# Kernel tuning notes

Measured on AMD Instinct MI355X. Metric: run time of the kernel, lower is better.

The kernel has to match this reference:

```python
import jax, jax.numpy as jnp
import numpy as np

C = 1.0          # curvature args.c
ALPHA = 3.0      # self.alpha
MIN = 1e-15      # min_norm clamp (HGCN PoincareBall)
PROJ_EPS = 4e-3  # fp32 boundary eps (HGCN)


def _norm(x):
    return jnp.maximum(jnp.linalg.norm(x, axis=-1, keepdims=True), MIN)


def artanh(x):
    # clamp for fp32 stability (HGCN clamps to 1 - 1e-15; 1e-7 is the fp32 analogue)
    return jnp.arctanh(jnp.clip(x, -1.0 + 1e-7, 1.0 - 1e-7))


def proj(x, c):
    n = _norm(x)
    maxn = (1.0 - PROJ_EPS) / jnp.sqrt(c)
    return jnp.where(n > maxn, x / n * maxn, x)


def expmap0(u, c):
    sc = jnp.sqrt(c)
    n = _norm(u)
    return jnp.tanh(sc * n) * u / (sc * n)


def logmap0(p, c):
    sc = jnp.sqrt(c)
    n = _norm(p)
    return artanh(sc * n) * p / (sc * n)


def mobius_add(x, y, c):
    x2 = jnp.sum(x * x, axis=-1, keepdims=True)
    y2 = jnp.sum(y * y, axis=-1, keepdims=True)
    xy = jnp.sum(x * y, axis=-1, keepdims=True)
    num = (1.0 + 2.0 * c * xy + c * y2) * x + (1.0 - c * x2) * y
    den = 1.0 + 2.0 * c * xy + c * c * x2 * y2
    return num / jnp.maximum(den, MIN)


def mobius_matvec(m, x, c):
    sc = jnp.sqrt(c)
    xn = _norm(x)
    mx = x @ m.T                      # [..., out]
    mxn = _norm(mx)
    res = jnp.tanh(mxn / xn * artanh(sc * xn)) * mx / (mxn * sc)
    zero_rows = jnp.all(mx == 0.0, axis=-1, keepdims=True)
    return jnp.where(zero_rows, 0.0, res)


def hyp_linear(x, W, b, c):
    # dropout on weights is identity in eval mode
    mv = proj(mobius_matvec(W, x, c), c)
    hb = proj(expmap0(b[None, :], c), c)  # proj_tan0 is identity on Poincare ball
    return proj(mobius_add(mv, hb, c), c)


def setup_inputs() -> dict:
    key = jax.random.key(0)
    N, D, F = 8192, 128, 128
    ks = jax.random.split(key, 8)
    gain = np.sqrt(2.0 / (D + D)) * np.sqrt(2.0)  # xavier-like scale
    return {
        "idx": jnp.arange(N, dtype=jnp.int32),
        "dist_metrix": jnp.zeros((1,), dtype=jnp.float32),
        "x": jax.random.normal(ks[0], (N, F), dtype=jnp.float32),
        "emb1": jax.random.normal(ks[1], (N, D), dtype=jnp.float32),
        "emb2": jax.random.normal(ks[2], (N, D), dtype=jnp.float32),
        "W1": jax.random.normal(ks[3], (D, D), dtype=jnp.float32) * gain,
        "b1": jax.random.normal(ks[4], (D,), dtype=jnp.float32) * 0.01,
        "W2": jax.random.normal(ks[5], (D, D), dtype=jnp.float32) * gain,
        "b2": jax.random.normal(ks[6], (D,), dtype=jnp.float32) * 0.01,
    }


def reference(idx, dist_metrix, x, emb1, emb2, W1, b1, W2, b2):
    # node embeddings lifted to the Poincare ball (proj_tan0 is identity)
    nv1 = proj(expmap0(emb1[idx], C), C)
    nv2 = proj(expmap0(emb2[idx], C), C)
    nv1 = hyp_linear(nv1, W1, b1, C)
    nv2 = hyp_linear(nv2, W2, b2, C)
    # adjacency construction: a1 = nv2 @ nv1^T (mobius), a2 = nv1 @ nv2^T (mobius)
    a1 = mobius_matvec(nv1, nv2, C)   # [N, N]
    a2 = mobius_matvec(nv2, nv1, C)   # [N, N]
    a = mobius_add(a1, -a2, C)
    adj = jax.nn.relu(jnp.tanh(ALPHA * a))
    n = adj.shape[0]
    adj = adj + 1e-4 * jnp.eye(n, dtype=adj.dtype)
    # row-normalize (scipy round-trip in original == row-sum divide, inf -> 0)
    rs = jnp.sum(adj, axis=1, keepdims=True)
    adj = adj * jnp.where(rs == 0.0, 0.0, 1.0 / rs)
    # propagate features
    xt = logmap0(x, C)                       # [N, F]
    out = mobius_matvec(xt.T, adj, C)        # adj @ xt -> [N, F]
    out = logmap0(out, C)
    return out
```

## Files before the change

kernel.cpp:

```cpp
#include <hip/hip_runtime.h>
#include <hip/hip_bf16.h>


typedef __attribute__((ext_vector_type(8))) short short8;
typedef __attribute__((ext_vector_type(4))) float f32x4;

#define MAXN 0.996f

__device__ __forceinline__ float artanh_clip(float x) {
    x = fminf(x, 1.0f - 1e-7f);
    x = fmaxf(x, -1.0f + 1e-7f);
    return 0.5f * logf((1.0f + x) / (1.0f - x));
}

__device__ __forceinline__ float red8(float v) {
    v += __shfl_xor(v, 1);
    v += __shfl_xor(v, 2);
    v += __shfl_xor(v, 4);
    return v;
}

__device__ __forceinline__ float red64(float v) {
#pragma unroll
    for (int m = 1; m < 64; m <<= 1) v += __shfl_xor(v, m);
    return v;
}

__device__ __forceinline__ unsigned short f2bf(float f) {
    __hip_bfloat16 h = __float2bfloat16(f);
    return *reinterpret_cast<unsigned short*>(&h);
}

__device__ __forceinline__ float bf2f(unsigned short u) {
    __hip_bfloat16 h;
    *reinterpret_cast<unsigned short*>(&h) = u;
    return __bfloat162float(h);
}

__global__ void hb_kernel(const float* __restrict__ b1, const float* __restrict__ b2,
                          float* __restrict__ hbws) {
    const int l = threadIdx.x;
    for (int which = 0; which < 2; ++which) {
        const float* b = which ? b2 : b1;
        float e0 = b[l], e1 = b[l + 64];
        float n = fmaxf(sqrtf(red64(e0 * e0 + e1 * e1)), 1e-15f);
        float th = tanhf(n);
        float s0 = th / n;
        float u0 = e0 * s0, u1 = e1 * s0;
        float nu = fmaxf(sqrtf(red64(u0 * u0 + u1 * u1)), 1e-15f);
        float ps = (nu > MAXN) ? MAXN / nu : 1.0f;
        float h0 = u0 * ps, h1 = u1 * ps;
        float y2 = red64(h0 * h0 + h1 * h1);
        hbws[which * 128 + l] = h0;
        hbws[which * 128 + l + 64] = h1;
        if (l == 0) hbws[256 + which] = y2;
    }
}

__global__ __launch_bounds__(256) void prep_kernel(
    const int* __restrict__ idx,
    const float* __restrict__ emb1, const float* __restrict__ emb2,
    const float* __restrict__ W1, const float* __restrict__ W2,
    const float* __restrict__ hbws,
    unsigned short* __restrict__ nv1b, unsigned short* __restrict__ nv2b,
    float* __restrict__ xn1, float* __restrict__ xn2) {
    __shared__ __align__(16) float uL[32 * 132];
    __shared__ float mxL[32 * 132];
    __shared__ float xnL[32];
    __shared__ float hbL[128];

    const int which = blockIdx.y;
    const float* emb = which ? emb2 : emb1;
    const float* W = which ? W2 : W1;
    unsigned short* nvb = which ? nv2b : nv1b;
    float* xno = which ? xn2 : xn1;
    const float y2 = hbws[256 + which];

    const int tid = threadIdx.x;
    const int rblk = blockIdx.x * 32;
    if (tid < 128) hbL[tid] = hbws[which * 128 + tid];

    const int r = tid >> 3, s = tid & 7;
    const int row = rblk + r;
    const int src = idx[row];
    float ev[16];
    float p2 = 0.f;
#pragma unroll
    for (int kk = 0; kk < 16; ++kk) {
        float e = emb[src * 128 + s + kk * 8];
        ev[kk] = e;
        p2 += e * e;
    }
    float n2 = red8(p2);
    float n = fmaxf(sqrtf(n2), 1e-15f);
    float th = tanhf(n);
    float nu = fmaxf(th, 1e-15f);
    float ps = (nu > MAXN) ? (MAXN / nu) : 1.0f;
    float sc0 = (th / n) * ps;
#pragma unroll
    for (int kk = 0; kk < 16; ++kk) uL[r * 132 + s + kk * 8] = ev[kk] * sc0;
    if (s == 0) xnL[r] = fmaxf(nu * ps, 1e-15f);
    __syncthreads();

    const int o = tid & 127, rb = tid >> 7;
    float mxv[16];
#pragma unroll
    for (int rr = 0; rr < 16; ++rr) mxv[rr] = 0.f;
    for (int k4 = 0; k4 < 128; k4 += 4) {
        const float4 wv = *reinterpret_cast<const float4*>(&W[o * 128 + k4]);
#pragma unroll
        for (int rr = 0; rr < 16; ++rr) {
            const float4 uv = *reinterpret_cast<const float4*>(&uL[(rb + rr * 2) * 132 + k4]);
            mxv[rr] += uv.x * wv.x + uv.y * wv.y + uv.z * wv.z + uv.w * wv.w;
        }
    }
#pragma unroll
    for (int rr = 0; rr < 16; ++rr) mxL[(rb + rr * 2) * 132 + o] = mxv[rr];
    __syncthreads();

    float mx[16];
    float m2 = 0.f;
#pragma unroll
    for (int kk = 0; kk < 16; ++kk) {
        mx[kk] = mxL[r * 132 + s + kk * 8];
        m2 += mx[kk] * mx[kk];
    }
    float mxn = fmaxf(sqrtf(red8(m2)), 1e-15f);
    float xnv = xnL[r];
    float tt = tanhf(mxn / xnv * artanh_clip(xnv));
    float nres = fmaxf(tt, 1e-15f);
    float ps2 = (nres > MAXN) ? (MAXN / nres) : 1.0f;
    float s2 = (tt / mxn) * ps2;
    float mvn = nres * ps2;
    float x2 = mvn * mvn;
    float xyp = 0.f;
    float mv[16];
#pragma unroll
    for (int kk = 0; kk < 16; ++kk) {
        mv[kk] = mx[kk] * s2;
        xyp += mv[kk] * hbL[s + kk * 8];
    }
    float xy = red8(xyp);
    float cA = 1.f + 2.f * xy + y2;
    float cB = 1.f - x2;
    float rden = 1.f / fmaxf(1.f + 2.f * xy + x2 * y2, 1e-15f);
    float r2v[16];
    float q2 = 0.f;
#pragma unroll
    for (int kk = 0; kk < 16; ++kk) {
        float v = (cA * mv[kk] + cB * hbL[s + kk * 8]) * rden;
        r2v[kk] = v;
        q2 += v * v;
    }
    float nr2 = fmaxf(sqrtf(red8(q2)), 1e-15f);
    float ps3 = (nr2 > MAXN) ? (MAXN / nr2) : 1.0f;
#pragma unroll
    for (int kk = 0; kk < 16; ++kk) nvb[row * 128 + s + kk * 8] = f2bf(r2v[kk] * ps3);
    if (s == 0) xno[row] = fmaxf((nr2 > MAXN) ? MAXN : nr2, 1e-15f);
}

__global__ __launch_bounds__(256) void xt_kernel(const float* __restrict__ x,
                                                 unsigned short* __restrict__ xtT) {
    __shared__ float xv[32 * 132];
    const int tid = threadIdx.x;
    const int rblk = blockIdx.x * 32;
    const int r = tid >> 3, s = tid & 7;
    float ev[16];
    float p2 = 0.f;
#pragma unroll
    for (int kk = 0; kk < 16; ++kk) {
        float e = x[(rblk + r) * 128 + s + kk * 8];
        ev[kk] = e;
        p2 += e * e;
    }
    const float n = fmaxf(sqrtf(red8(p2)), 1e-15f);
    const float scl = artanh_clip(n) / n;
#pragma unroll
    for (int kk = 0; kk < 16; ++kk) xv[r * 132 + s + kk * 8] = ev[kk] * scl;
    __syncthreads();
    const int k = tid >> 1, h = tid & 1;
    short8 o0, o1;
#pragma unroll
    for (int j = 0; j < 8; ++j) o0[j] = (short)f2bf(xv[(h * 16 + j) * 132 + k]);
#pragma unroll
    for (int j = 0; j < 8; ++j) o1[j] = (short)f2bf(xv[(h * 16 + 8 + j) * 132 + k]);
    *reinterpret_cast<short8*>(&xtT[k * 8192 + rblk + h * 16]) = o0;
    *reinterpret_cast<short8*>(&xtT[k * 8192 + rblk + h * 16 + 8]) = o1;
}

__global__ __launch_bounds__(256) void gram_kernel(const unsigned short* __restrict__ nv1b,
                                                   const unsigned short* __restrict__ nv2b,
                                                   float* __restrict__ G) {
    __shared__ float Ab[64 * 33], Bb[64 * 33];
    const int tile = blockIdx.x, mat = blockIdx.y, kc = blockIdx.z;
    const int ta = (tile & 3) * 32, tb = (tile >> 2) * 32;
    const unsigned short* Am = (mat == 1) ? nv2b : nv1b;
    const unsigned short* Bm = (mat == 0) ? nv1b : nv2b;
    const int tid = threadIdx.x;
    const int oa = tid & 31, obb = (tid >> 5) * 4;
    float acc[4] = {0.f, 0.f, 0.f, 0.f};
    for (int sc = 0; sc < 16; ++sc) {
        const int r0 = kc * 1024 + sc * 64;
        for (int i0 = tid; i0 < 2048; i0 += 256) {
            int rr = i0 >> 5, cc = i0 & 31;
            Ab[rr * 33 + cc] = bf2f(Am[(r0 + rr) * 128 + ta + cc]);
            Bb[rr * 33 + cc] = bf2f(Bm[(r0 + rr) * 128 + tb + cc]);
        }
        __syncthreads();
#pragma unroll 4
        for (int rr = 0; rr < 64; ++rr) {
            float av = Ab[rr * 33 + oa];
#pragma unroll
            for (int i = 0; i < 4; ++i) acc[i] += av * Bb[rr * 33 + obb + i];
        }
        __syncthreads();
    }
#pragma unroll
    for (int i = 0; i < 4; ++i)
        atomicAdd(&G[mat * 16384 + (ta + oa) * 128 + tb + obb + i], acc[i]);
}

__global__ __launch_bounds__(256) void rowcoef_kernel(
    const float* __restrict__ G, const float* __restrict__ xn1, const float* __restrict__ xn2,
    const unsigned short* __restrict__ nv1b, const unsigned short* __restrict__ nv2b,
    float* __restrict__ P, float* __restrict__ Q) {
    __shared__ __align__(16) float v1L[32 * 132];
    __shared__ __align__(16) float v2L[32 * 132];
    __shared__ float tL[32 * 132];
    __shared__ float RCX[3][32];
    const int tid = threadIdx.x;
    const int rblk = blockIdx.x * 32;
    for (int i = tid; i < 4096; i += 256) {
        int r = i >> 7, c = i & 127;
        v1L[r * 132 + c] = bf2f(nv1b[(rblk + r) * 128 + c]);
        v2L[r * 132 + c] = bf2f(nv2b[(rblk + r) * 128 + c]);
    }
    __syncthreads();
    const int o = tid & 127, rb = tid >> 7;
    const int rA = tid >> 3, sA = tid & 7;
    for (int mat = 0; mat < 3; ++mat) {
        const float* vR = (mat == 0) ? v2L : v1L;
        const float* vL = (mat == 1) ? v1L : v2L;
        const float* Gm = G + mat * 16384;
        float tv[16];
#pragma unroll
        for (int rr = 0; rr < 16; ++rr) tv[rr] = 0.f;
        for (int k4 = 0; k4 < 128; k4 += 4) {
            const float4 gv = *reinterpret_cast<const float4*>(&Gm[o * 128 + k4]);
#pragma unroll
            for (int rr = 0; rr < 16; ++rr) {
                const float4 uv = *reinterpret_cast<const float4*>(&vR[(rb + rr * 2) * 132 + k4]);
                tv[rr] += uv.x * gv.x + uv.y * gv.y + uv.z * gv.z + uv.w * gv.w;
            }
        }
        __syncthreads();
#pragma unroll
        for (int rr = 0; rr < 16; ++rr) {
            int rw = rb + rr * 2;
            tL[rw * 132 + o] = vL[rw * 132 + o] * tv[rr];
        }
        __syncthreads();
        float p = 0.f;
#pragma unroll
        for (int kk = 0; kk < 16; ++kk) p += tL[rA * 132 + sA + kk * 8];
        p = red8(p);
        if (sA == 0) RCX[mat][rA] = p;
    }
    __syncthreads();
    if (tid < 32) {
        const int row = rblk + tid;
        const float R = RCX[0][tid], Cc = RCX[1][tid], X = RCX[2][tid];
        const float xn1v = xn1[row], xn2v = xn2[row];
        const float mxn1 = fmaxf(sqrtf(fmaxf(R, 0.f)), 1e-15f);
        const float t1 = tanhf(mxn1 / xn2v * artanh_clip(xn2v));
        const float f1 = t1 / mxn1;
        const float mxn2 = fmaxf(sqrtf(fmaxf(Cc, 0.f)), 1e-15f);
        const float t2 = tanhf(mxn2 / xn1v * artanh_clip(xn1v));
        const float f2 = t2 / mxn2;
        const float x2 = f1 * f1 * R, y2 = f2 * f2 * Cc;
        const float xy = -f1 * f2 * X;
        const float rden = 1.f / fmaxf(1.f + 2.f * xy + x2 * y2, 1e-15f);
        P[row] = (1.f + 2.f * xy + y2) * f1 * rden;
        Q[row] = -(1.f - x2) * f2 * rden;
    }
}

__global__ __launch_bounds__(512) void fused_kernel(
    const unsigned short* __restrict__ nv1b, const unsigned short* __restrict__ nv2b,
    const unsigned short* __restrict__ xtT,
    const float* __restrict__ P, const float* __restrict__ Q,
    float* __restrict__ U, float* __restrict__ rs, float* __restrict__ qs) {
    __shared__ float S1[32 * 132];
    __shared__ float S2[128 * 33];
    __shared__ __align__(16) unsigned short adjb[32 * 136];
    __shared__ float PL[32], QL[32];
    __shared__ int s2flag;

    const int tid = threadIdx.x;
    const int w = tid >> 6, l = tid & 63;
    const int iblk = blockIdx.x * 32;

    if (tid == 0) s2flag = 0;
    if (tid < 32) {
        PL[tid] = P[iblk + tid];
        QL[tid] = Q[iblk + tid];
    }
    __syncthreads();
    if (tid < 32 && fabsf(QL[tid]) > 1e-6f) atomicOr(&s2flag, 1);
    __syncthreads();
    const bool needS2 = (s2flag != 0);

    short8 areg[2][4];
#pragma unroll
    for (int tr = 0; tr < 2; ++tr)
#pragma unroll
        for (int kk = 0; kk < 4; ++kk)
            areg[tr][kk] = *reinterpret_cast<const short8*>(
                &nv2b[(iblk + tr * 16 + (l & 15)) * 128 + kk * 32 + (l >> 4) * 8]);

    const f32x4 zero4 = {0.f, 0.f, 0.f, 0.f};
    f32x4 accU[2];
    accU[0] = zero4;
    accU[1] = zero4;
    float rsA[4] = {0.f, 0.f, 0.f, 0.f};
    float qA[4] = {0.f, 0.f, 0.f, 0.f};

    auto computeS1 = [&](int jb) {
        const int jblk = jb * 128;
        f32x4 acc0 = zero4, acc1 = zero4;
#pragma unroll
        for (int kk = 0; kk < 4; ++kk) {
            short8 b = *reinterpret_cast<const short8*>(
                &nv1b[(jblk + w * 16 + (l & 15)) * 128 + kk * 32 + (l >> 4) * 8]);
            acc0 = __builtin_amdgcn_mfma_f32_16x16x32_bf16(areg[0][kk], b, acc0, 0, 0, 0);
            acc1 = __builtin_amdgcn_mfma_f32_16x16x32_bf16(areg[1][kk], b, acc1, 0, 0, 0);
        }
#pragma unroll
        for (int v = 0; v < 4; ++v) {
            S1[((l >> 4) * 4 + v) * 132 + w * 16 + (l & 15)] = acc0[v];
            S1[(16 + (l >> 4) * 4 + v) * 132 + w * 16 + (l & 15)] = acc1[v];
        }
        if (needS2) {
            f32x4 a20 = zero4, a21 = zero4;
#pragma unroll
            for (int kk = 0; kk < 4; ++kk) {
                short8 a2 = *reinterpret_cast<const short8*>(
                    &nv2b[(jblk + w * 16 + (l & 15)) * 128 + kk * 32 + (l >> 4) * 8]);
                short8 b20 = *reinterpret_cast<const short8*>(
                    &nv1b[(iblk + (l & 15)) * 128 + kk * 32 + (l >> 4) * 8]);
                short8 b21 = *reinterpret_cast<const short8*>(
                    &nv1b[(iblk + 16 + (l & 15)) * 128 + kk * 32 + (l >> 4) * 8]);
                a20 = __builtin_amdgcn_mfma_f32_16x16x32_bf16(a2, b20, a20, 0, 0, 0);
                a21 = __builtin_amdgcn_mfma_f32_16x16x32_bf16(a2, b21, a21, 0, 0, 0);
            }
#pragma unroll
            for (int v = 0; v < 4; ++v) {
                S2[(w * 16 + (l >> 4) * 4 + v) * 33 + (l & 15)] = a20[v];
                S2[(w * 16 + (l >> 4) * 4 + v) * 33 + 16 + (l & 15)] = a21[v];
            }
        }
    };

    computeS1(0);
    for (int jb = 0; jb < 64; ++jb) {
        const int jblk = jb * 128;
        __syncthreads();
#pragma unroll
        for (int k = 0; k < 4; ++k) {
            const int r = w + 8 * k;
            const float Pv = PL[r], Qv = QL[r];
#pragma unroll
            for (int h = 0; h < 2; ++h) {
                const int c = l + 64 * h;
                float a = Pv * S1[r * 132 + c];
                if (needS2) a += Qv * S2[c * 33 + r];
                float e = __expf(fminf(6.0f * a, 60.0f));
                float t = 1.0f - 2.0f / (e + 1.0f);
                float ad = (a > 0.0f) ? t : 0.0f;
                if (iblk + r == jblk + c) ad += 1e-4f;
                rsA[k] += ad;
                qA[k] += ad * ad;
                adjb[r * 136 + c] = f2bf(ad);
            }
        }
        __syncthreads();
#pragma unroll
        for (int kk = 0; kk < 4; ++kk) {
            short8 b = *reinterpret_cast<const short8*>(
                &xtT[(w * 16 + (l & 15)) * 8192 + jblk + kk * 32 + (l >> 4) * 8]);
#pragma unroll
            for (int tr = 0; tr < 2; ++tr) {
                short8 a = *reinterpret_cast<const short8*>(
                    &adjb[(tr * 16 + (l & 15)) * 136 + kk * 32 + (l >> 4) * 8]);
                accU[tr] = __builtin_amdgcn_mfma_f32_16x16x32_bf16(a, b, accU[tr], 0, 0, 0);
            }
        }
        if (jb + 1 < 64) computeS1(jb + 1);
    }

#pragma unroll
    for (int tr = 0; tr < 2; ++tr)
#pragma unroll
        for (int v = 0; v < 4; ++v)
            U[(iblk + tr * 16 + (l >> 4) * 4 + v) * 128 + w * 16 + (l & 15)] = accU[tr][v];
#pragma unroll
    for (int k = 0; k < 4; ++k) {
        float rsv = red64(rsA[k]);
        float qv = red64(qA[k]);
        if (l == 0) {
            rs[iblk + w + 8 * k] = rsv;
            qs[iblk + w + 8 * k] = qv;
        }
    }
}

__global__ void finalize_kernel(const float* __restrict__ U, const float* __restrict__ rs,
                                const float* __restrict__ qs, float* __restrict__ out) {
    const int row = blockIdx.x, l = threadIdx.x;
    const float u0 = U[row * 128 + l], u1 = U[row * 128 + 64 + l];
    const float rsv = rs[row];
    const float wv = (rsv == 0.f) ? 0.f : 1.f / rsv;
    const float m0 = u0 * wv, m1 = u1 * wv;
    const float mxn = fmaxf(sqrtf(red64(m0 * m0 + m1 * m1)), 1e-15f);
    const float xn = fmaxf(sqrtf(fmaxf(qs[row], 0.f)) * wv, 1e-15f);
    const float tt = tanhf(mxn / xn * artanh_clip(xn));
    const float nres = fmaxf(tt, 1e-15f);
    const float lsc = (tt / mxn) * (artanh_clip(nres) / nres);
    out[row * 128 + l] = m0 * lsc;
    out[row * 128 + 64 + l] = m1 * lsc;
}

extern "C" void kernel_launch(void* const* d_in, const int* in_sizes, int n_in,
                              void* d_out, int out_size, void* d_ws, size_t ws_size,
                              hipStream_t stream) {
    const int* idx = (const int*)d_in[0];
    const float* x = (const float*)d_in[2];
    const float* emb1 = (const float*)d_in[3];
    const float* emb2 = (const float*)d_in[4];
    const float* W1 = (const float*)d_in[5];
    const float* b1 = (const float*)d_in[6];
    const float* W2 = (const float*)d_in[7];
    const float* b2 = (const float*)d_in[8];
    float* out = (float*)d_out;
    char* ws = (char*)d_ws;

    unsigned short* nv1b = (unsigned short*)(ws + 0x000000);
    unsigned short* nv2b = (unsigned short*)(ws + 0x200000);
    unsigned short* xtT = (unsigned short*)(ws + 0x400000);
    float* G = (float*)(ws + 0x600000);
    float* hbws = (float*)(ws + 0x630000);
    float* xn1 = (float*)(ws + 0x630600);
    float* xn2 = (float*)(ws + 0x638600);
    float* P = (float*)(ws + 0x640600);
    float* Q = (float*)(ws + 0x648600);
    float* rs = (float*)(ws + 0x650600);
    float* qs = (float*)(ws + 0x658600);
    float* U = out;

    hipMemsetAsync(G, 0, 3 * 128 * 128 * sizeof(float), stream);
    hb_kernel<<<1, 64, 0, stream>>>(b1, b2, hbws);
    prep_kernel<<<dim3(256, 2), 256, 0, stream>>>(idx, emb1, emb2, W1, W2, hbws,
                                                  nv1b, nv2b, xn1, xn2);
    xt_kernel<<<256, 256, 0, stream>>>(x, xtT);
    gram_kernel<<<dim3(16, 3, 8), 256, 0, stream>>>(nv1b, nv2b, G);
    rowcoef_kernel<<<256, 256, 0, stream>>>(G, xn1, xn2, nv1b, nv2b, P, Q);
    fused_kernel<<<256, 512, 0, stream>>>(nv1b, nv2b, xtT, P, Q, U, rs, qs);
    finalize_kernel<<<8192, 64, 0, stream>>>(U, rs, qs, out);
    (void)in_sizes; (void)n_in; (void)out_size; (void)ws_size; (void)d_in;
}
```

Before: 400.5 us.

## Split fused adjacency kernel over column blocks and prescale nv2 by P

The fused adjacency-propagation kernel now runs on a 256x4 grid, with each block covering 16 of the 64 column blocks. Partial U, row-sum and square-sum results are combined with atomicAdd into buffers that are zeroed by memsets first. The row coefficient P is folded into a prescaled bf16 copy of nv2 built in rowcoef, so the inner loop drops one multiply. The Q term is merged into S1 directly instead of going through a separate S2 buffer, which frees shared memory. The tanh/relu is now computed with exp2 and rcp intrinsics, and the diagonal test only runs on diagonal tiles. The aim is to fill more of the GPU with 1024 blocks instead of 256, at the price of atomics, extra memsets, and an extra bf16 rounding of P*nv2.

```diff
diff --git a/kernel.cpp b/kernel.cpp
--- a/kernel.cpp
+++ b/kernel.cpp
@@ -223,11 +223,12 @@
 __global__ __launch_bounds__(256) void rowcoef_kernel(
     const float* __restrict__ G, const float* __restrict__ xn1, const float* __restrict__ xn2,
     const unsigned short* __restrict__ nv1b, const unsigned short* __restrict__ nv2b,
-    float* __restrict__ P, float* __restrict__ Q) {
+    float* __restrict__ P, float* __restrict__ Q, unsigned short* __restrict__ nv2p) {
     __shared__ __align__(16) float v1L[32 * 132];
     __shared__ __align__(16) float v2L[32 * 132];
     __shared__ float tL[32 * 132];
     __shared__ float RCX[3][32];
+    __shared__ float PshL[32];
     const int tid = threadIdx.x;
     const int rblk = blockIdx.x * 32;
     for (int i = tid; i < 4096; i += 256) {
@@ -280,31 +281,35 @@
         const float x2 = f1 * f1 * R, y2 = f2 * f2 * Cc;
         const float xy = -f1 * f2 * X;
         const float rden = 1.f / fmaxf(1.f + 2.f * xy + x2 * y2, 1e-15f);
-        P[row] = (1.f + 2.f * xy + y2) * f1 * rden;
+        const float Pv = (1.f + 2.f * xy + y2) * f1 * rden;
+        P[row] = Pv;
+        PshL[tid] = Pv;
         Q[row] = -(1.f - x2) * f2 * rden;
     }
-}
-
-__global__ __launch_bounds__(512) void fused_kernel(
-    const unsigned short* __restrict__ nv1b, const unsigned short* __restrict__ nv2b,
-    const unsigned short* __restrict__ xtT,
-    const float* __restrict__ P, const float* __restrict__ Q,
+    __syncthreads();
+    for (int i = tid; i < 4096; i += 256) {
+        int r = i >> 7, c = i & 127;
+        nv2p[(rblk + r) * 128 + c] = f2bf(PshL[r] * v2L[r * 132 + c]);
+    }
+}
+
+__global__ __launch_bounds__(512, 8) void fused_kernel(
+    const unsigned short* __restrict__ nv1b, const unsigned short* __restrict__ nv2p,
+    const unsigned short* __restrict__ nv2b, const unsigned short* __restrict__ xtT,
+    const float* __restrict__ Q,
     float* __restrict__ U, float* __restrict__ rs, float* __restrict__ qs) {
     __shared__ float S1[32 * 132];
-    __shared__ float S2[128 * 33];
     __shared__ __align__(16) unsigned short adjb[32 * 136];
-    __shared__ float PL[32], QL[32];
+    __shared__ float QL[32];
     __shared__ int s2flag;
 
     const int tid = threadIdx.x;
     const int w = tid >> 6, l = tid & 63;
     const int iblk = blockIdx.x * 32;
+    const int jb0 = blockIdx.y * 16;
 
     if (tid == 0) s2flag = 0;
-    if (tid < 32) {
-        PL[tid] = P[iblk + tid];
-        QL[tid] = Q[iblk + tid];
-    }
+    if (tid < 32) QL[tid] = Q[iblk + tid];
     __syncthreads();
     if (tid < 32 && fabsf(QL[tid]) > 1e-6f) atomicOr(&s2flag, 1);
     __syncthreads();
@@ -316,7 +321,7 @@
 #pragma unroll
         for (int kk = 0; kk < 4; ++kk)
             areg[tr][kk] = *reinterpret_cast<const short8*>(
-                &nv2b[(iblk + tr * 16 + (l & 15)) * 128 + kk * 32 + (l >> 4) * 8]);
+                &nv2p[(iblk + tr * 16 + (l & 15)) * 128 + kk * 32 + (l >> 4) * 8]);
 
     const f32x4 zero4 = {0.f, 0.f, 0.f, 0.f};
     f32x4 accU[2];
@@ -340,49 +345,58 @@
             S1[((l >> 4) * 4 + v) * 132 + w * 16 + (l & 15)] = acc0[v];
             S1[(16 + (l >> 4) * 4 + v) * 132 + w * 16 + (l & 15)] = acc1[v];
         }
+    };
+
+    auto s2merge = [&](int jb) {
+        const int jblk = jb * 128;
+        f32x4 a20 = zero4, a21 = zero4;
+#pragma unroll
+        for (int kk = 0; kk < 4; ++kk) {
+            short8 a2 = *reinterpret_cast<const short8*>(
+                &nv2b[(jblk + w * 16 + (l & 15)) * 128 + kk * 32 + (l >> 4) * 8]);
+            short8 b20 = *reinterpret_cast<const short8*>(
+                &nv1b[(iblk + (l & 15)) * 128 + kk * 32 + (l >> 4) * 8]);
+            short8 b21 = *reinterpret_cast<const short8*>(
+                &nv1b[(iblk + 16 + (l & 15)) * 128 + kk * 32 + (l >> 4) * 8]);
+            a20 = __builtin_amdgcn_mfma_f32_16x16x32_bf16(a2, b20, a20, 0, 0, 0);
+            a21 = __builtin_amdgcn_mfma_f32_16x16x32_bf16(a2, b21, a21, 0, 0, 0);
+        }
+        const int jloc = w * 16 + (l >> 4) * 4;
+        const int i0 = l & 15;
+#pragma unroll
+        for (int v = 0; v < 4; ++v) {
+            S1[i0 * 132 + jloc + v] += QL[i0] * a20[v];
+            S1[(i0 + 16) * 132 + jloc + v] += QL[i0 + 16] * a21[v];
+        }
+    };
+
+    computeS1(jb0);
+    for (int jb = jb0; jb < jb0 + 16; ++jb) {
+        const int jblk = jb * 128;
+        __syncthreads();
         if (needS2) {
-            f32x4 a20 = zero4, a21 = zero4;
-#pragma unroll
-            for (int kk = 0; kk < 4; ++kk) {
-                short8 a2 = *reinterpret_cast<const short8*>(
-                    &nv2b[(jblk + w * 16 + (l & 15)) * 128 + kk * 32 + (l >> 4) * 8]);
-                short8 b20 = *reinterpret_cast<const short8*>(
-                    &nv1b[(iblk + (l & 15)) * 128 + kk * 32 + (l >> 4) * 8]);
-                short8 b21 = *reinterpret_cast<const short8*>(
-                    &nv1b[(iblk + 16 + (l & 15)) * 128 + kk * 32 + (l >> 4) * 8]);
-                a20 = __builtin_amdgcn_mfma_f32_16x16x32_bf16(a2, b20, a20, 0, 0, 0);
-                a21 = __builtin_amdgcn_mfma_f32_16x16x32_bf16(a2, b21, a21, 0, 0, 0);
+            s2merge(jb);
+            __syncthreads();
+        }
+        auto adjLoop = [&](bool dodiag) {
+#pragma unroll
+            for (int k = 0; k < 4; ++k) {
+                const int r = w + 8 * k;
+#pragma unroll
+                for (int h = 0; h < 2; ++h) {
+                    const int c = l + 64 * h;
+                    float a = S1[r * 132 + c];
+                    float e = __builtin_amdgcn_exp2f(a * 8.65617025f);
+                    float t = 1.0f - 2.0f * __builtin_amdgcn_rcpf(e + 1.0f);
+                    float ad = fmaxf(t, 0.0f);
+                    if (dodiag && (iblk + r == jblk + c)) ad += 1e-4f;
+                    rsA[k] += ad;
+                    qA[k] += ad * ad;
+                    adjb[r * 136 + c] = f2bf(ad);
+                }
             }
-#pragma unroll
-            for (int v = 0; v < 4; ++v) {
-                S2[(w * 16 + (l >> 4) * 4 + v) * 33 + (l & 15)] = a20[v];
-                S2[(w * 16 + (l >> 4) * 4 + v) * 33 + 16 + (l & 15)] = a21[v];
-            }
-        }
-    };
-
-    computeS1(0);
-    for (int jb = 0; jb < 64; ++jb) {
-        const int jblk = jb * 128;
-        __syncthreads();
-#pragma unroll
-        for (int k = 0; k < 4; ++k) {
-            const int r = w + 8 * k;
-            const float Pv = PL[r], Qv = QL[r];
-#pragma unroll
-            for (int h = 0; h < 2; ++h) {
-                const int c = l + 64 * h;
-                float a = Pv * S1[r * 132 + c];
-                if (needS2) a += Qv * S2[c * 33 + r];
-                float e = __expf(fminf(6.0f * a, 60.0f));
-                float t = 1.0f - 2.0f / (e + 1.0f);
-                float ad = (a > 0.0f) ? t : 0.0f;
-                if (iblk + r == jblk + c) ad += 1e-4f;
-                rsA[k] += ad;
-                qA[k] += ad * ad;
-                adjb[r * 136 + c] = f2bf(ad);
-            }
-        }
+        };
+        if ((unsigned)(iblk - jblk) < 128u) adjLoop(true); else adjLoop(false);
         __syncthreads();
 #pragma unroll
         for (int kk = 0; kk < 4; ++kk) {
@@ -395,21 +409,22 @@
                 accU[tr] = __builtin_amdgcn_mfma_f32_16x16x32_bf16(a, b, accU[tr], 0, 0, 0);
             }
         }
-        if (jb + 1 < 64) computeS1(jb + 1);
+        if (jb + 1 < jb0 + 16) computeS1(jb + 1);
     }
 
 #pragma unroll
     for (int tr = 0; tr < 2; ++tr)
 #pragma unroll
         for (int v = 0; v < 4; ++v)
-            U[(iblk + tr * 16 + (l >> 4) * 4 + v) * 128 + w * 16 + (l & 15)] = accU[tr][v];
+            atomicAdd(&U[(iblk + tr * 16 + (l >> 4) * 4 + v) * 128 + w * 16 + (l & 15)],
+                      accU[tr][v]);
 #pragma unroll
     for (int k = 0; k < 4; ++k) {
         float rsv = red64(rsA[k]);
         float qv = red64(qA[k]);
         if (l == 0) {
-            rs[iblk + w + 8 * k] = rsv;
-            qs[iblk + w + 8 * k] = qv;
+            atomicAdd(&rs[iblk + w + 8 * k], rsv);
+            atomicAdd(&qs[iblk + w + 8 * k], qv);
         }
     }
 }
@@ -447,24 +462,28 @@
     unsigned short* nv1b = (unsigned short*)(ws + 0x000000);
     unsigned short* nv2b = (unsigned short*)(ws + 0x200000);
     unsigned short* xtT = (unsigned short*)(ws + 0x400000);
-    float* G = (float*)(ws + 0x600000);
-    float* hbws = (float*)(ws + 0x630000);
-    float* xn1 = (float*)(ws + 0x630600);
-    float* xn2 = (float*)(ws + 0x638600);
-    float* P = (float*)(ws + 0x640600);
-    float* Q = (float*)(ws + 0x648600);
-    float* rs = (float*)(ws + 0x650600);
-    float* qs = (float*)(ws + 0x658600);
+    unsigned short* nv2p = (unsigned short*)(ws + 0x600000);
+    float* G = (float*)(ws + 0x800000);
+    float* hbws = (float*)(ws + 0x830000);
+    float* xn1 = (float*)(ws + 0x831000);
+    float* xn2 = (float*)(ws + 0x839000);
+    float* P = (float*)(ws + 0x841000);
+    float* Q = (float*)(ws + 0x849000);
+    float* rs = (float*)(ws + 0x851000);
+    float* qs = (float*)(ws + 0x859000);
     float* U = out;
 
     hipMemsetAsync(G, 0, 3 * 128 * 128 * sizeof(float), stream);
+    hipMemsetAsync(rs, 0, 8192 * sizeof(float), stream);
+    hipMemsetAsync(qs, 0, 8192 * sizeof(float), stream);
+    hipMemsetAsync(U, 0, 8192 * 128 * sizeof(float), stream);
     hb_kernel<<<1, 64, 0, stream>>>(b1, b2, hbws);
     prep_kernel<<<dim3(256, 2), 256, 0, stream>>>(idx, emb1, emb2, W1, W2, hbws,
                                                   nv1b, nv2b, xn1, xn2);
     xt_kernel<<<256, 256, 0, stream>>>(x, xtT);
     gram_kernel<<<dim3(16, 3, 8), 256, 0, stream>>>(nv1b, nv2b, G);
-    rowcoef_kernel<<<256, 256, 0, stream>>>(G, xn1, xn2, nv1b, nv2b, P, Q);
-    fused_kernel<<<256, 512, 0, stream>>>(nv1b, nv2b, xtT, P, Q, U, rs, qs);
+    rowcoef_kernel<<<256, 256, 0, stream>>>(G, xn1, xn2, nv1b, nv2b, P, Q, nv2p);
+    fused_kernel<<<dim3(256, 4), 512, 0, stream>>>(nv1b, nv2p, nv2b, xtT, Q, U, rs, qs);
     finalize_kernel<<<8192, 64, 0, stream>>>(U, rs, qs, out);
     (void)in_sizes; (void)n_in; (void)out_size; (void)ws_size; (void)d_in;
 }
```

Result: slower. 453.9 us (+13.3%).
